# Performance work log

Measured on AMD Instinct MI355X. Metric: run time of the kernel, lower is better.

Reference implementation:

```python
import jax, jax.numpy as jnp
import numpy as np

B, S, D = 256, 512, 128
NQ, NC, NQD, NCD = 20000, 2000, 101, 101


def setup_inputs() -> dict:
    key = jax.random.key(0)
    ks = jax.random.split(key, 32)
    s = 0.05
    inp = {
        "question_seq": jax.random.randint(ks[0], (B, S), 0, NQ),
        "concept_seq": jax.random.randint(ks[1], (B, S), 0, NC),
        "question_diff_seq": jax.random.randint(ks[2], (B, S), 0, NQD),
        "concept_diff_seq": jax.random.randint(ks[3], (B, S), 0, NCD),
        "correct_seq": jax.random.randint(ks[4], (B, S), 0, 2),
        "E_q": jax.random.normal(ks[5], (NQ, D)) * s,
        "E_c": jax.random.normal(ks[6], (NC, D)) * s,
        "E_qd": jax.random.normal(ks[7], (NQD, D)) * s,
        "E_cd": jax.random.normal(ks[8], (NCD, D)) * s,
        "E_corr": jax.random.normal(ks[9], (2, D)) * s,
        "Wx": jax.random.normal(ks[10], (4 * D, D)) * s,
        "bx": jnp.zeros((D,)),
        "W_s1": jax.random.normal(ks[11], (D, D)) * s,
        "b_s1": jnp.zeros((D,)),
        "W_s2": jax.random.normal(ks[12], (D, D)) * s,
        "b_s2": jnp.zeros((D,)),
        "W_p1": jax.random.normal(ks[13], (2 * D, D)) * s,
        "b_p1": jnp.zeros((D,)),
        "W_p2": jax.random.normal(ks[14], (2 * D, D)) * s,
        "b_p2": jnp.zeros((D,)),
        "W_ki": jax.random.normal(ks[15], (4 * D, D)) * s,
        "b_ki": jnp.zeros((D,)),
        # xavier_uniform init of h_pre: bound = sqrt(6/(fan_in+fan_out))
        "h0": jax.random.uniform(ks[16], (B, D), minval=-1.0, maxval=1.0) * np.sqrt(6.0 / (B + D)),
    }
    return inp


def reference(question_seq, concept_seq, question_diff_seq, concept_diff_seq,
              correct_seq, E_q, E_c, E_qd, E_cd, E_corr,
              Wx, bx, W_s1, b_s1, W_s2, b_s2,
              W_p1, b_p1, W_p2, b_p2, W_ki, b_ki, h0):
    # embedding lookups: [B,S,D] each
    q = E_q[question_seq]
    c = E_c[concept_seq]
    qd = E_qd[question_diff_seq]
    cd = E_cd[concept_diff_seq]
    corr = E_corr[correct_seq]
    # generate_x_MLP applied to full sequence at once (loop-invariant)
    x = jnp.concatenate([q, c, qd, cd], axis=-1) @ Wx + bx  # [B,S,D]
    # time-major inputs for the recurrence over t = 0..S-2
    xs = jnp.swapaxes(x, 0, 1)          # [S,B,D]
    corr_t = jnp.swapaxes(corr, 0, 1)   # [S,B,D]
    qd_t = jnp.swapaxes(qd, 0, 1)
    cd_t = jnp.swapaxes(cd, 0, 1)

    def step(h, inp):
        x_t, x_next, co, qdt, cdt = inp
        d = x_t - h
        sdf = jax.nn.sigmoid(d @ W_s1 + b_s1) * jnp.tanh(d @ W_s2 + b_s2)  # dropout=eval
        pk_in = jnp.concatenate([sdf, co], axis=-1)
        pka = jax.nn.sigmoid(pk_in @ W_p1 + b_p1) * jnp.tanh(pk_in @ W_p2 + b_p2)
        ki_in = jnp.concatenate([h, co, qdt, cdt], axis=-1)
        g = jax.nn.sigmoid(ki_in @ W_ki + b_ki)
        h_new = g * h + (1.0 - g) * pka
        y_t = jax.nn.sigmoid(jnp.sum(x_next * h_new, axis=-1))  # [B]
        return h_new, y_t

    scan_in = (xs[:-1], xs[1:], corr_t[:-1], qd_t[:-1], cd_t[:-1])
    _, y_body = jax.lax.scan(step, h0, scan_in)  # y_body: [S-1,B]
    y = jnp.concatenate([y_body.T, jnp.zeros((question_seq.shape[0], 1), y_body.dtype)], axis=1)
    return y  # [B,S], last column zero as in original
```

## Files before the change

kernel.cpp:

```cpp
#include <hip/hip_runtime.h>

#define BB 256
#define SS 512
#define DD 128

__device__ __forceinline__ float sigf(float v) {
    return __builtin_amdgcn_rcpf(1.0f + __expf(-v));
}
__device__ __forceinline__ float tanhf_(float v) {
    return 1.0f - 2.0f * __builtin_amdgcn_rcpf(__expf(2.0f * v) + 1.0f);
}

typedef _Float16 f16x2 __attribute__((ext_vector_type(2)));
typedef _Float16 f16x8 __attribute__((ext_vector_type(8)));
typedef float    f32x4 __attribute__((ext_vector_type(4)));

#define MFMA16(A, B, C) __builtin_amdgcn_mfma_f32_16x16x32_f16((A), (B), (C), 0, 0, 0)

#define N_EQ  (20000 * 128)
#define N_EC  (2000 * 128)
#define N_EQD (101 * 128)
#define N_ECD (101 * 128)
#define N_WXT (512 * 128)
#define N_CVT (N_EQ + N_EC + N_EQD + N_ECD + N_WXT)

__global__ __launch_bounds__(256) void dimkt_cvt(
    const float* __restrict__ E_q, const float* __restrict__ E_c,
    const float* __restrict__ E_qd, const float* __restrict__ E_cd,
    const float* __restrict__ Wx,
    _Float16* __restrict__ E_qh, _Float16* __restrict__ E_ch,
    _Float16* __restrict__ E_qdh, _Float16* __restrict__ E_cdh,
    _Float16* __restrict__ WxTh)
{
    int o = blockIdx.x * 256 + threadIdx.x;
    if (o >= N_CVT) return;
    if (o < N_EQ) { E_qh[o] = (_Float16)E_q[o]; return; }
    o -= N_EQ;
    if (o < N_EC) { E_ch[o] = (_Float16)E_c[o]; return; }
    o -= N_EC;
    if (o < N_EQD) { E_qdh[o] = (_Float16)E_qd[o]; return; }
    o -= N_EQD;
    if (o < N_ECD) { E_cdh[o] = (_Float16)E_cd[o]; return; }
    o -= N_ECD;
    int n = o >> 9, k = o & 511;
    WxTh[o] = (_Float16)Wx[k * 128 + n];
}

__global__ void dimkt_tables(const float* __restrict__ E_corr,
                             const float* __restrict__ E_qd,
                             const float* __restrict__ E_cd,
                             const float* __restrict__ W_ki,
                             const float* __restrict__ W_p1,
                             const float* __restrict__ W_p2,
                             const float* __restrict__ b_ki,
                             const float* __restrict__ b_p1,
                             const float* __restrict__ b_p2,
                             float* __restrict__ Ck, float* __restrict__ Cp1,
                             float* __restrict__ Cp2, float* __restrict__ Qk,
                             float* __restrict__ Cdk)
{
    __shared__ float e[128];
    const int r = blockIdx.x;
    const int j = threadIdx.x;
    const float *emb, *W, *bias;
    float* op;
    if (r < 2)        { emb = E_corr + r * 128;        W = W_ki + 128 * 128; bias = b_ki;    op = Ck  + r * 128; }
    else if (r < 4)   { emb = E_corr + (r - 2) * 128;  W = W_p1 + 128 * 128; bias = b_p1;    op = Cp1 + (r - 2) * 128; }
    else if (r < 6)   { emb = E_corr + (r - 4) * 128;  W = W_p2 + 128 * 128; bias = b_p2;    op = Cp2 + (r - 4) * 128; }
    else if (r < 107) { emb = E_qd   + (r - 6) * 128;  W = W_ki + 256 * 128; bias = nullptr; op = Qk  + (r - 6) * 128; }
    else              { emb = E_cd   + (r - 107) * 128; W = W_ki + 384 * 128; bias = nullptr; op = Cdk + (r - 107) * 128; }
    e[j] = emb[j];
    __syncthreads();
    float acc = bias ? bias[j] : 0.0f;
#pragma unroll 8
    for (int i = 0; i < 128; ++i) acc = fmaf(e[i], W[i * 128 + j], acc);
    op[j] = acc;
}

__global__ __launch_bounds__(256, 2) void dimkt_xgemm(
    const int* __restrict__ q_seq, const int* __restrict__ c_seq,
    const int* __restrict__ qd_seq, const int* __restrict__ cd_seq,
    const _Float16* __restrict__ E_qh, const _Float16* __restrict__ E_ch,
    const _Float16* __restrict__ E_qdh, const _Float16* __restrict__ E_cdh,
    const _Float16* __restrict__ WxTh,
    const float* __restrict__ bx, float* __restrict__ xout)
{
    const int tid = threadIdx.x;
    const int wv  = tid >> 6;
    const int l   = tid & 63;
    const int lm  = l & 15;
    const int kg8 = (l >> 4) * 8;
    const int m0  = blockIdx.x * 128;
    const int rbase = m0 + wv * 32;

    f32x4 acc0[8], acc1[8];
#pragma unroll
    for (int c = 0; c < 8; ++c) {
        acc0[c] = (f32x4){0.f, 0.f, 0.f, 0.f};
        acc1[c] = (f32x4){0.f, 0.f, 0.f, 0.f};
    }

#pragma unroll
    for (int s = 0; s < 4; ++s) {
        const _Float16* T  = (s == 0) ? E_qh : (s == 1) ? E_ch : (s == 2) ? E_qdh : E_cdh;
        const int*      sq = (s == 0) ? q_seq : (s == 1) ? c_seq : (s == 2) ? qd_seq : cd_seq;
        const int i0 = sq[rbase + lm];
        const int i1 = sq[rbase + 16 + lm];
        const _Float16* a0p = T + (size_t)i0 * 128 + kg8;
        const _Float16* a1p = T + (size_t)i1 * 128 + kg8;
#pragma unroll
        for (int kk = 0; kk < 4; ++kk) {
            const f16x8 a0 = *(const f16x8*)(a0p + kk * 32);
            const f16x8 a1 = *(const f16x8*)(a1p + kk * 32);
#pragma unroll
            for (int c = 0; c < 8; ++c) {
                const f16x8 bf = *(const f16x8*)&WxTh[(size_t)(c * 16 + lm) * 512
                                                      + s * 128 + kk * 32 + kg8];
                acc0[c] = MFMA16(a0, bf, acc0[c]);
                acc1[c] = MFMA16(a1, bf, acc1[c]);
            }
        }
    }

#pragma unroll
    for (int c = 0; c < 8; ++c) {
        const int col = c * 16 + lm;
        const float bxv = bx[col];
#pragma unroll
        for (int r = 0; r < 4; ++r) {
            const int row0 = rbase + (l >> 4) * 4 + r;
            xout[(size_t)row0 * 128 + col]        = acc0[c][r] + bxv;
            xout[(size_t)(row0 + 16) * 128 + col] = acc1[c][r] + bxv;
        }
    }
}

__device__ __forceinline__ f16x8 load_wfrag(const float* __restrict__ W,
                                            int kbase, int j) {
    f16x8 r;
#pragma unroll
    for (int e = 0; e < 8; ++e) r[e] = (_Float16)W[(kbase + e) * DD + j];
    return r;
}

__global__ __launch_bounds__(512, 2) void dimkt_scan(
    const float* __restrict__ x,
    const int* __restrict__ corr_seq, const int* __restrict__ qd_seq,
    const int* __restrict__ cd_seq,
    const float* __restrict__ W_s1, const float* __restrict__ b_s1,
    const float* __restrict__ W_s2, const float* __restrict__ b_s2,
    const float* __restrict__ W_p1, const float* __restrict__ W_p2,
    const float* __restrict__ W_ki,
    const float* __restrict__ Ck, const float* __restrict__ Cp1,
    const float* __restrict__ Cp2, const float* __restrict__ Qk,
    const float* __restrict__ Cdk,
    const float* __restrict__ h0, _Float16* __restrict__ hb,
    float* __restrict__ out)
{
    __shared__ __align__(16) _Float16 d_h[128];
    __shared__ __align__(16) _Float16 h_h[128];
    __shared__ __align__(16) _Float16 s_h[128];

    const int tid  = threadIdx.x;
    const int b    = blockIdx.x;
    const int wv   = tid >> 6;
    const int l    = tid & 63;
    const int kgrp = l >> 4;
    const int j    = wv * 16 + (l & 15);
    const int base = b * SS;

    const int kb = kgrp * 8;
    const f16x8 w1f0 = load_wfrag(W_s1,  0 + kb, j);
    const f16x8 w1f1 = load_wfrag(W_s1, 32 + kb, j);
    const f16x8 w1f2 = load_wfrag(W_s1, 64 + kb, j);
    const f16x8 w1f3 = load_wfrag(W_s1, 96 + kb, j);
    const f16x8 w2f0 = load_wfrag(W_s2,  0 + kb, j);
    const f16x8 w2f1 = load_wfrag(W_s2, 32 + kb, j);
    const f16x8 w2f2 = load_wfrag(W_s2, 64 + kb, j);
    const f16x8 w2f3 = load_wfrag(W_s2, 96 + kb, j);
    const f16x8 wkf0 = load_wfrag(W_ki,  0 + kb, j);
    const f16x8 wkf1 = load_wfrag(W_ki, 32 + kb, j);
    const f16x8 wkf2 = load_wfrag(W_ki, 64 + kb, j);
    const f16x8 wkf3 = load_wfrag(W_ki, 96 + kb, j);
    const f16x8 p1f0 = load_wfrag(W_p1,  0 + kb, j);
    const f16x8 p1f1 = load_wfrag(W_p1, 32 + kb, j);
    const f16x8 p1f2 = load_wfrag(W_p1, 64 + kb, j);
    const f16x8 p1f3 = load_wfrag(W_p1, 96 + kb, j);
    const f16x8 p2f0 = load_wfrag(W_p2,  0 + kb, j);
    const f16x8 p2f1 = load_wfrag(W_p2, 32 + kb, j);
    const f16x8 p2f2 = load_wfrag(W_p2, 64 + kb, j);
    const f16x8 p2f3 = load_wfrag(W_p2, 96 + kb, j);

    const float bs1 = b_s1[j];
    const float bs2 = b_s2[j];
    float h  = h0[b * DD + j];
    float x0 = x[(size_t)base * DD + j];
    if (kgrp == 0) {
        h_h[j] = (_Float16)h;
        d_h[j] = (_Float16)(x0 - h);
    }
    {
        int ic0 = corr_seq[base], iq0 = qd_seq[base], ie0 = cd_seq[base];
        float a = Ck [ic0 * DD + j];  float q = Qk [iq0 * DD + j];
        float c = Cdk[ie0 * DD + j];  float p = Cp1[ic0 * DD + j];
        float p2v = Cp2[ic0 * DD + j];
        (void)a; (void)q; (void)c; (void)p; (void)p2v;
    }
    int ic0 = corr_seq[base], iq0 = qd_seq[base], ie0 = cd_seq[base];
    float tck = Ck [ic0 * DD + j];
    float tqk = Qk [iq0 * DD + j];
    float tcd = Cdk[ie0 * DD + j];
    float tp1 = Cp1[ic0 * DD + j];
    float tp2 = Cp2[ic0 * DD + j];
    int icN = corr_seq[base + 1], iqN = qd_seq[base + 1], ieN = cd_seq[base + 1];
    float xn  = x[(size_t)(base + 1) * DD + j];
    __syncthreads();

    for (int t = 0; t < 511; ++t) {
        float nck = Ck [icN * DD + j];
        float nqk = Qk [iqN * DD + j];
        float ncd = Cdk[ieN * DD + j];
        float np1 = Cp1[icN * DD + j];
        float np2 = Cp2[icN * DD + j];
        const int n2 = base + ((t + 2 > 511) ? 511 : (t + 2));
        int icN2 = corr_seq[n2], iqN2 = qd_seq[n2], ieN2 = cd_seq[n2];
        int xp = (t + 2 > 511) ? 511 : (t + 2);
        float xnn = x[(size_t)(base + xp) * DD + j];

        const f16x8 dA0 = *(const f16x8*)&d_h[ 0 + kb];
        const f16x8 dA1 = *(const f16x8*)&d_h[32 + kb];
        const f16x8 dA2 = *(const f16x8*)&d_h[64 + kb];
        const f16x8 dA3 = *(const f16x8*)&d_h[96 + kb];
        const f16x8 hA0 = *(const f16x8*)&h_h[ 0 + kb];
        const f16x8 hA1 = *(const f16x8*)&h_h[32 + kb];
        const f16x8 hA2 = *(const f16x8*)&h_h[64 + kb];
        const f16x8 hA3 = *(const f16x8*)&h_h[96 + kb];

        const f32x4 z = {0.f, 0.f, 0.f, 0.f};
        f32x4 c1a = MFMA16(dA0, w1f0, z);
        f32x4 c2a = MFMA16(dA0, w2f0, z);
        f32x4 cka = MFMA16(hA0, wkf0, z);
        f32x4 c1b = MFMA16(dA2, w1f2, z);
        f32x4 c2b = MFMA16(dA2, w2f2, z);
        f32x4 ckb = MFMA16(hA2, wkf2, z);
        c1a = MFMA16(dA1, w1f1, c1a);
        c2a = MFMA16(dA1, w2f1, c2a);
        cka = MFMA16(hA1, wkf1, cka);
        c1b = MFMA16(dA3, w1f3, c1b);
        c2b = MFMA16(dA3, w2f3, c2b);
        ckb = MFMA16(hA3, wkf3, ckb);

        float sdf = sigf(c1a[0] + c1b[0] + bs1) * tanhf_(c2a[0] + c2b[0] + bs2);
        float g   = sigf(cka[0] + ckb[0] + tck + tqk + tcd);
        if (kgrp == 0) s_h[j] = (_Float16)sdf;
        __syncthreads();

        const f16x8 sA0 = *(const f16x8*)&s_h[ 0 + kb];
        const f16x8 sA1 = *(const f16x8*)&s_h[32 + kb];
        const f16x8 sA2 = *(const f16x8*)&s_h[64 + kb];
        const f16x8 sA3 = *(const f16x8*)&s_h[96 + kb];

        f32x4 q1a = MFMA16(sA0, p1f0, z);
        f32x4 q2a = MFMA16(sA0, p2f0, z);
        f32x4 q1b = MFMA16(sA2, p1f2, z);
        f32x4 q2b = MFMA16(sA2, p2f2, z);
        q1a = MFMA16(sA1, p1f1, q1a);
        q2a = MFMA16(sA1, p2f1, q2a);
        q1b = MFMA16(sA3, p1f3, q1b);
        q2b = MFMA16(sA3, p2f3, q2b);

        float pka = sigf(q1a[0] + q1b[0] + tp1) * tanhf_(q2a[0] + q2b[0] + tp2);
        float hn  = g * h + (1.f - g) * pka;
        _Float16 hn16 = (_Float16)hn;
        if (kgrp == 0) {
            h_h[j] = hn16;
            d_h[j] = (_Float16)(xn - hn);
            hb[(size_t)(base + t) * DD + j] = hn16;
        }

        h = hn; xn = xnn;
        tck = nck; tqk = nqk; tcd = ncd; tp1 = np1; tp2 = np2;
        icN = icN2; iqN = iqN2; ieN = ieN2;
        __syncthreads();
    }

    if (tid == 0) out[base + 511] = 0.0f;
}

__global__ __launch_bounds__(256) void dimkt_y(
    const float* __restrict__ x, const _Float16* __restrict__ hb,
    float* __restrict__ out)
{
    const int o = blockIdx.x * 4 + (threadIdx.x >> 6);
    const int l = threadIdx.x & 63;
    const int b = o >> 9;
    const int t = o & 511;
    if (t == 511) return;
    float2 xv = *(const float2*)&x[((size_t)(b * SS + t + 1)) * DD + 2 * l];
    f16x2  hv = *(const f16x2*)&hb[((size_t)(b * SS + t)) * DD + 2 * l];
    float s = xv.x * (float)hv.x + xv.y * (float)hv.y;
    s += __shfl_xor(s, 1);  s += __shfl_xor(s, 2);  s += __shfl_xor(s, 4);
    s += __shfl_xor(s, 8);  s += __shfl_xor(s, 16); s += __shfl_xor(s, 32);
    if (l == 0) out[b * SS + t] = sigf(s);
}

extern "C" void kernel_launch(void* const* d_in, const int* in_sizes, int n_in,
                              void* d_out, int out_size, void* d_ws, size_t ws_size,
                              hipStream_t stream) {
    const int*   q_seq    = (const int*)d_in[0];
    const int*   c_seq    = (const int*)d_in[1];
    const int*   qd_seq   = (const int*)d_in[2];
    const int*   cd_seq   = (const int*)d_in[3];
    const int*   corr_seq = (const int*)d_in[4];
    const float* E_q    = (const float*)d_in[5];
    const float* E_c    = (const float*)d_in[6];
    const float* E_qd   = (const float*)d_in[7];
    const float* E_cd   = (const float*)d_in[8];
    const float* E_corr = (const float*)d_in[9];
    const float* Wx     = (const float*)d_in[10];
    const float* bx     = (const float*)d_in[11];
    const float* W_s1   = (const float*)d_in[12];
    const float* b_s1   = (const float*)d_in[13];
    const float* W_s2   = (const float*)d_in[14];
    const float* b_s2   = (const float*)d_in[15];
    const float* W_p1   = (const float*)d_in[16];
    const float* b_p1   = (const float*)d_in[17];
    const float* W_p2   = (const float*)d_in[18];
    const float* b_p2   = (const float*)d_in[19];
    const float* W_ki   = (const float*)d_in[20];
    const float* b_ki   = (const float*)d_in[21];
    const float* h0     = (const float*)d_in[22];
    float* out = (float*)d_out;

    float* xbuf = (float*)d_ws;
    float* Ck   = xbuf + (size_t)BB * SS * DD;
    float* Cp1  = Ck  + 256;
    float* Cp2  = Cp1 + 256;
    float* Qk   = Cp2 + 256;
    float* Cdk  = Qk  + 101 * 128;
    _Float16* pool  = (_Float16*)(xbuf + 16804864);
    _Float16* hbuf  = pool;
    _Float16* E_qh  = hbuf + (size_t)BB * SS * DD;
    _Float16* E_ch  = E_qh + N_EQ;
    _Float16* E_qdh = E_ch + N_EC;
    _Float16* E_cdh = E_qdh + N_EQD;
    _Float16* WxTh  = E_cdh + N_ECD;

    dimkt_cvt<<<(N_CVT + 255) / 256, 256, 0, stream>>>(
        E_q, E_c, E_qd, E_cd, Wx, E_qh, E_ch, E_qdh, E_cdh, WxTh);

    dimkt_tables<<<208, 128, 0, stream>>>(E_corr, E_qd, E_cd, W_ki, W_p1, W_p2,
                                          b_ki, b_p1, b_p2, Ck, Cp1, Cp2, Qk, Cdk);

    dimkt_xgemm<<<(BB * SS) / 128, 256, 0, stream>>>(q_seq, c_seq, qd_seq, cd_seq,
                                                     E_qh, E_ch, E_qdh, E_cdh,
                                                     WxTh, bx, xbuf);

    dimkt_scan<<<BB, 512, 0, stream>>>(xbuf, corr_seq, qd_seq, cd_seq,
                                       W_s1, b_s1, W_s2, b_s2, W_p1, W_p2, W_ki,
                                       Ck, Cp1, Cp2, Qk, Cdk, h0, hbuf, out);

    dimkt_y<<<(BB * SS) / 4, 256, 0, stream>>>(xbuf, hbuf, out);
}
```

Before: 521.1 us.

## Hoist x@W_s1 and x@W_s2 out of the recurrence into a batched GEMM

Uses linearity (x_t - h)@W = x_t@W - h@W to precompute x@W_s1+b and x@W_s2+b for all timesteps in a new MFMA GEMM kernel. The scan loop then reuses the h fragments for the s1/s2 MFMAs and no longer builds a separate d operand in LDS. x is also stored as fp16 to halve traffic, and sequence indices are made wave-uniform with readfirstlane. This adds an extra kernel and two [B*S*D] fp16 buffers, and lowers the precision of x.

```diff
diff --git a/kernel.cpp b/kernel.cpp
--- a/kernel.cpp
+++ b/kernel.cpp
@@ -22,15 +22,18 @@
 #define N_EQD (101 * 128)
 #define N_ECD (101 * 128)
 #define N_WXT (512 * 128)
-#define N_CVT (N_EQ + N_EC + N_EQD + N_ECD + N_WXT)
+#define N_WS  (128 * 128)
+#define N_CVT (N_EQ + N_EC + N_EQD + N_ECD + N_WXT + 2 * N_WS)
 
 __global__ __launch_bounds__(256) void dimkt_cvt(
     const float* __restrict__ E_q, const float* __restrict__ E_c,
     const float* __restrict__ E_qd, const float* __restrict__ E_cd,
     const float* __restrict__ Wx,
+    const float* __restrict__ W_s1, const float* __restrict__ W_s2,
     _Float16* __restrict__ E_qh, _Float16* __restrict__ E_ch,
     _Float16* __restrict__ E_qdh, _Float16* __restrict__ E_cdh,
-    _Float16* __restrict__ WxTh)
+    _Float16* __restrict__ WxTh,
+    _Float16* __restrict__ Ws1T, _Float16* __restrict__ Ws2T)
 {
     int o = blockIdx.x * 256 + threadIdx.x;
     if (o >= N_CVT) return;
@@ -42,8 +45,22 @@
     o -= N_EQD;
     if (o < N_ECD) { E_cdh[o] = (_Float16)E_cd[o]; return; }
     o -= N_ECD;
-    int n = o >> 9, k = o & 511;
-    WxTh[o] = (_Float16)Wx[k * 128 + n];
+    if (o < N_WXT) {
+        int n = o >> 9, k = o & 511;
+        WxTh[o] = (_Float16)Wx[k * 128 + n];
+        return;
+    }
+    o -= N_WXT;
+    if (o < N_WS) {
+        int n = o >> 7, k = o & 127;
+        Ws1T[o] = (_Float16)W_s1[k * 128 + n];
+        return;
+    }
+    o -= N_WS;
+    {
+        int n = o >> 7, k = o & 127;
+        Ws2T[o] = (_Float16)W_s2[k * 128 + n];
+    }
 }
 
 __global__ void dimkt_tables(const float* __restrict__ E_corr,
@@ -83,7 +100,7 @@
     const _Float16* __restrict__ E_qh, const _Float16* __restrict__ E_ch,
     const _Float16* __restrict__ E_qdh, const _Float16* __restrict__ E_cdh,
     const _Float16* __restrict__ WxTh,
-    const float* __restrict__ bx, float* __restrict__ xout)
+    const float* __restrict__ bx, _Float16* __restrict__ xh)
 {
     const int tid = threadIdx.x;
     const int wv  = tid >> 6;
@@ -129,8 +146,58 @@
 #pragma unroll
         for (int r = 0; r < 4; ++r) {
             const int row0 = rbase + (l >> 4) * 4 + r;
-            xout[(size_t)row0 * 128 + col]        = acc0[c][r] + bxv;
-            xout[(size_t)(row0 + 16) * 128 + col] = acc1[c][r] + bxv;
+            xh[(size_t)row0 * 128 + col]        = (_Float16)(acc0[c][r] + bxv);
+            xh[(size_t)(row0 + 16) * 128 + col] = (_Float16)(acc1[c][r] + bxv);
+        }
+    }
+}
+
+__global__ __launch_bounds__(256, 2) void dimkt_x12(
+    const _Float16* __restrict__ xh,
+    const _Float16* __restrict__ Ws1T, const _Float16* __restrict__ Ws2T,
+    const float* __restrict__ b_s1, const float* __restrict__ b_s2,
+    _Float16* __restrict__ X1h, _Float16* __restrict__ X2h)
+{
+    const int tid = threadIdx.x;
+    const int wv  = tid >> 6;
+    const int l   = tid & 63;
+    const int lm  = l & 15;
+    const int kg8 = (l >> 4) * 8;
+    const int rbase = blockIdx.x * 128 + wv * 32;
+
+    f32x4 acc0[16], acc1[16];
+#pragma unroll
+    for (int c = 0; c < 16; ++c) {
+        acc0[c] = (f32x4){0.f, 0.f, 0.f, 0.f};
+        acc1[c] = (f32x4){0.f, 0.f, 0.f, 0.f};
+    }
+
+    const _Float16* a0p = xh + (size_t)(rbase + lm) * 128 + kg8;
+    const _Float16* a1p = xh + (size_t)(rbase + 16 + lm) * 128 + kg8;
+#pragma unroll
+    for (int kk = 0; kk < 4; ++kk) {
+        const f16x8 a0 = *(const f16x8*)(a0p + kk * 32);
+        const f16x8 a1 = *(const f16x8*)(a1p + kk * 32);
+#pragma unroll
+        for (int c = 0; c < 16; ++c) {
+            const _Float16* BT = (c < 8) ? Ws1T : Ws2T;
+            const f16x8 bf = *(const f16x8*)&BT[(size_t)((c & 7) * 16 + lm) * 128
+                                                + kk * 32 + kg8];
+            acc0[c] = MFMA16(a0, bf, acc0[c]);
+            acc1[c] = MFMA16(a1, bf, acc1[c]);
+        }
+    }
+
+#pragma unroll
+    for (int c = 0; c < 16; ++c) {
+        const int col = (c & 7) * 16 + lm;
+        const float bv = (c < 8) ? b_s1[col] : b_s2[col];
+        _Float16* ob = (c < 8) ? X1h : X2h;
+#pragma unroll
+        for (int r = 0; r < 4; ++r) {
+            const int row0 = rbase + (l >> 4) * 4 + r;
+            ob[(size_t)row0 * 128 + col]        = (_Float16)(acc0[c][r] + bv);
+            ob[(size_t)(row0 + 16) * 128 + col] = (_Float16)(acc1[c][r] + bv);
         }
     }
 }
@@ -144,11 +211,10 @@
 }
 
 __global__ __launch_bounds__(512, 2) void dimkt_scan(
-    const float* __restrict__ x,
+    const _Float16* __restrict__ X1h, const _Float16* __restrict__ X2h,
     const int* __restrict__ corr_seq, const int* __restrict__ qd_seq,
     const int* __restrict__ cd_seq,
-    const float* __restrict__ W_s1, const float* __restrict__ b_s1,
-    const float* __restrict__ W_s2, const float* __restrict__ b_s2,
+    const float* __restrict__ W_s1, const float* __restrict__ W_s2,
     const float* __restrict__ W_p1, const float* __restrict__ W_p2,
     const float* __restrict__ W_ki,
     const float* __restrict__ Ck, const float* __restrict__ Cp1,
@@ -157,7 +223,6 @@
     const float* __restrict__ h0, _Float16* __restrict__ hb,
     float* __restrict__ out)
 {
-    __shared__ __align__(16) _Float16 d_h[128];
     __shared__ __align__(16) _Float16 h_h[128];
     __shared__ __align__(16) _Float16 s_h[128];
 
@@ -191,29 +256,22 @@
     const f16x8 p2f2 = load_wfrag(W_p2, 64 + kb, j);
     const f16x8 p2f3 = load_wfrag(W_p2, 96 + kb, j);
 
-    const float bs1 = b_s1[j];
-    const float bs2 = b_s2[j];
-    float h  = h0[b * DD + j];
-    float x0 = x[(size_t)base * DD + j];
-    if (kgrp == 0) {
-        h_h[j] = (_Float16)h;
-        d_h[j] = (_Float16)(x0 - h);
-    }
-    {
-        int ic0 = corr_seq[base], iq0 = qd_seq[base], ie0 = cd_seq[base];
-        float a = Ck [ic0 * DD + j];  float q = Qk [iq0 * DD + j];
-        float c = Cdk[ie0 * DD + j];  float p = Cp1[ic0 * DD + j];
-        float p2v = Cp2[ic0 * DD + j];
-        (void)a; (void)q; (void)c; (void)p; (void)p2v;
-    }
-    int ic0 = corr_seq[base], iq0 = qd_seq[base], ie0 = cd_seq[base];
-    float tck = Ck [ic0 * DD + j];
-    float tqk = Qk [iq0 * DD + j];
-    float tcd = Cdk[ie0 * DD + j];
-    float tp1 = Cp1[ic0 * DD + j];
-    float tp2 = Cp2[ic0 * DD + j];
-    int icN = corr_seq[base + 1], iqN = qd_seq[base + 1], ieN = cd_seq[base + 1];
-    float xn  = x[(size_t)(base + 1) * DD + j];
+    float h = h0[b * DD + j];
+    if (kgrp == 0) h_h[j] = (_Float16)h;
+
+    int ic = __builtin_amdgcn_readfirstlane(corr_seq[base]);
+    int iq = __builtin_amdgcn_readfirstlane(qd_seq[base]);
+    int ie = __builtin_amdgcn_readfirstlane(cd_seq[base]);
+    float tck = Ck [ic * DD + j];
+    float tqk = Qk [iq * DD + j];
+    float tcd = Cdk[ie * DD + j];
+    float tp1 = Cp1[ic * DD + j];
+    float tp2 = Cp2[ic * DD + j];
+    int icN = __builtin_amdgcn_readfirstlane(corr_seq[base + 1]);
+    int iqN = __builtin_amdgcn_readfirstlane(qd_seq[base + 1]);
+    int ieN = __builtin_amdgcn_readfirstlane(cd_seq[base + 1]);
+    float X1v = (float)X1h[(size_t)base * DD + j];
+    float X2v = (float)X2h[(size_t)base * DD + j];
     __syncthreads();
 
     for (int t = 0; t < 511; ++t) {
@@ -223,35 +281,36 @@
         float np1 = Cp1[icN * DD + j];
         float np2 = Cp2[icN * DD + j];
         const int n2 = base + ((t + 2 > 511) ? 511 : (t + 2));
-        int icN2 = corr_seq[n2], iqN2 = qd_seq[n2], ieN2 = cd_seq[n2];
-        int xp = (t + 2 > 511) ? 511 : (t + 2);
-        float xnn = x[(size_t)(base + xp) * DD + j];
-
-        const f16x8 dA0 = *(const f16x8*)&d_h[ 0 + kb];
-        const f16x8 dA1 = *(const f16x8*)&d_h[32 + kb];
-        const f16x8 dA2 = *(const f16x8*)&d_h[64 + kb];
-        const f16x8 dA3 = *(const f16x8*)&d_h[96 + kb];
+        int icN2 = __builtin_amdgcn_readfirstlane(corr_seq[n2]);
+        int iqN2 = __builtin_amdgcn_readfirstlane(qd_seq[n2]);
+        int ieN2 = __builtin_amdgcn_readfirstlane(cd_seq[n2]);
+        float nX1 = (float)X1h[(size_t)(base + t + 1) * DD + j];
+        float nX2 = (float)X2h[(size_t)(base + t + 1) * DD + j];
+
         const f16x8 hA0 = *(const f16x8*)&h_h[ 0 + kb];
         const f16x8 hA1 = *(const f16x8*)&h_h[32 + kb];
         const f16x8 hA2 = *(const f16x8*)&h_h[64 + kb];
         const f16x8 hA3 = *(const f16x8*)&h_h[96 + kb];
 
         const f32x4 z = {0.f, 0.f, 0.f, 0.f};
-        f32x4 c1a = MFMA16(dA0, w1f0, z);
-        f32x4 c2a = MFMA16(dA0, w2f0, z);
+        f32x4 c1a = MFMA16(hA0, w1f0, z);
+        f32x4 c2a = MFMA16(hA0, w2f0, z);
         f32x4 cka = MFMA16(hA0, wkf0, z);
-        f32x4 c1b = MFMA16(dA2, w1f2, z);
-        f32x4 c2b = MFMA16(dA2, w2f2, z);
+        f32x4 c1b = MFMA16(hA2, w1f2, z);
+        f32x4 c2b = MFMA16(hA2, w2f2, z);
         f32x4 ckb = MFMA16(hA2, wkf2, z);
-        c1a = MFMA16(dA1, w1f1, c1a);
-        c2a = MFMA16(dA1, w2f1, c2a);
+        c1a = MFMA16(hA1, w1f1, c1a);
+        c2a = MFMA16(hA1, w2f1, c2a);
         cka = MFMA16(hA1, wkf1, cka);
-        c1b = MFMA16(dA3, w1f3, c1b);
-        c2b = MFMA16(dA3, w2f3, c2b);
+        c1b = MFMA16(hA3, w1f3, c1b);
+        c2b = MFMA16(hA3, w2f3, c2b);
         ckb = MFMA16(hA3, wkf3, ckb);
 
-        float sdf = sigf(c1a[0] + c1b[0] + bs1) * tanhf_(c2a[0] + c2b[0] + bs2);
-        float g   = sigf(cka[0] + ckb[0] + tck + tqk + tcd);
+        float a1 = X1v - (c1a[0] + c1b[0]);
+        float a2 = X2v - (c2a[0] + c2b[0]);
+        float kg = cka[0] + ckb[0] + tck + tqk + tcd;
+        float sdf = sigf(a1) * tanhf_(a2);
+        float g   = sigf(kg);
         if (kgrp == 0) s_h[j] = (_Float16)sdf;
         __syncthreads();
 
@@ -270,15 +329,15 @@
         q2b = MFMA16(sA3, p2f3, q2b);
 
         float pka = sigf(q1a[0] + q1b[0] + tp1) * tanhf_(q2a[0] + q2b[0] + tp2);
-        float hn  = g * h + (1.f - g) * pka;
+        float hn  = fmaf(g, h - pka, pka);
         _Float16 hn16 = (_Float16)hn;
         if (kgrp == 0) {
             h_h[j] = hn16;
-            d_h[j] = (_Float16)(xn - hn);
             hb[(size_t)(base + t) * DD + j] = hn16;
         }
 
-        h = hn; xn = xnn;
+        h = hn;
+        X1v = nX1; X2v = nX2;
         tck = nck; tqk = nqk; tcd = ncd; tp1 = np1; tp2 = np2;
         icN = icN2; iqN = iqN2; ieN = ieN2;
         __syncthreads();
@@ -288,7 +347,7 @@
 }
 
 __global__ __launch_bounds__(256) void dimkt_y(
-    const float* __restrict__ x, const _Float16* __restrict__ hb,
+    const _Float16* __restrict__ xh, const _Float16* __restrict__ hb,
     float* __restrict__ out)
 {
     const int o = blockIdx.x * 4 + (threadIdx.x >> 6);
@@ -296,9 +355,9 @@
     const int b = o >> 9;
     const int t = o & 511;
     if (t == 511) return;
-    float2 xv = *(const float2*)&x[((size_t)(b * SS + t + 1)) * DD + 2 * l];
-    f16x2  hv = *(const f16x2*)&hb[((size_t)(b * SS + t)) * DD + 2 * l];
-    float s = xv.x * (float)hv.x + xv.y * (float)hv.y;
+    f16x2 xv = *(const f16x2*)&xh[((size_t)(b * SS + t + 1)) * DD + 2 * l];
+    f16x2 hv = *(const f16x2*)&hb[((size_t)(b * SS + t)) * DD + 2 * l];
+    float s = (float)xv.x * (float)hv.x + (float)xv.y * (float)hv.y;
     s += __shfl_xor(s, 1);  s += __shfl_xor(s, 2);  s += __shfl_xor(s, 4);
     s += __shfl_xor(s, 8);  s += __shfl_xor(s, 16); s += __shfl_xor(s, 32);
     if (l == 0) out[b * SS + t] = sigf(s);
@@ -332,33 +391,42 @@
     const float* h0     = (const float*)d_in[22];
     float* out = (float*)d_out;
 
-    float* xbuf = (float*)d_ws;
-    float* Ck   = xbuf + (size_t)BB * SS * DD;
+    float* Ck   = (float*)d_ws;
     float* Cp1  = Ck  + 256;
     float* Cp2  = Cp1 + 256;
     float* Qk   = Cp2 + 256;
     float* Cdk  = Qk  + 101 * 128;
-    _Float16* pool  = (_Float16*)(xbuf + 16804864);
-    _Float16* hbuf  = pool;
-    _Float16* E_qh  = hbuf + (size_t)BB * SS * DD;
+    _Float16* pool  = (_Float16*)((char*)d_ws + (size_t)131072);
+    const size_t NBT = (size_t)BB * SS * DD;
+    _Float16* xh    = pool;
+    _Float16* X1h   = xh  + NBT;
+    _Float16* X2h   = X1h + NBT;
+    _Float16* hbuf  = X2h + NBT;
+    _Float16* E_qh  = hbuf + NBT;
     _Float16* E_ch  = E_qh + N_EQ;
     _Float16* E_qdh = E_ch + N_EC;
     _Float16* E_cdh = E_qdh + N_EQD;
     _Float16* WxTh  = E_cdh + N_ECD;
+    _Float16* Ws1T  = WxTh + N_WXT;
+    _Float16* Ws2T  = Ws1T + N_WS;
 
     dimkt_cvt<<<(N_CVT + 255) / 256, 256, 0, stream>>>(
-        E_q, E_c, E_qd, E_cd, Wx, E_qh, E_ch, E_qdh, E_cdh, WxTh);
+        E_q, E_c, E_qd, E_cd, Wx, W_s1, W_s2,
+        E_qh, E_ch, E_qdh, E_cdh, WxTh, Ws1T, Ws2T);
 
     dimkt_tables<<<208, 128, 0, stream>>>(E_corr, E_qd, E_cd, W_ki, W_p1, W_p2,
                                           b_ki, b_p1, b_p2, Ck, Cp1, Cp2, Qk, Cdk);
 
     dimkt_xgemm<<<(BB * SS) / 128, 256, 0, stream>>>(q_seq, c_seq, qd_seq, cd_seq,
                                                      E_qh, E_ch, E_qdh, E_cdh,
-                                                     WxTh, bx, xbuf);
-
-    dimkt_scan<<<BB, 512, 0, stream>>>(xbuf, corr_seq, qd_seq, cd_seq,
-                                       W_s1, b_s1, W_s2, b_s2, W_p1, W_p2, W_ki,
+                                                     WxTh, bx, xh);
+
+    dimkt_x12<<<(BB * SS) / 128, 256, 0, stream>>>(xh, Ws1T, Ws2T, b_s1, b_s2,
+                                                   X1h, X2h);
+
+    dimkt_scan<<<BB, 512, 0, stream>>>(X1h, X2h, corr_seq, qd_seq, cd_seq,
+                                       W_s1, W_s2, W_p1, W_p2, W_ki,
                                        Ck, Cp1, Cp2, Qk, Cdk, h0, hbuf, out);
 
-    dimkt_y<<<(BB * SS) / 4, 256, 0, stream>>>(xbuf, hbuf, out);
-}
+    dimkt_y<<<(BB * SS) / 4, 256, 0, stream>>>(xh, hbuf, out);
+}
```

Result: slower. 565.6 us (+8.5%).
